# Optimization experiments

Measured on AMD Instinct MI355X. Metric: run time of the kernel, lower is better.

Reference implementation:

```python
import jax, jax.numpy as jnp
import numpy as np

EPS = 1e-8      # covariance regularizer (module-level `eps` in source repo)
ALPHA = 0.8     # style/content blend (module-level `alpha` in source repo)
SV_THRESH = 1e-5  # singular-value cutoff from the source


def _flatten(x):
    # x: [1, H, W, C] -> [C, H*W]
    xt = jnp.transpose(x[0], (2, 0, 1))  # C, H, W
    C = xt.shape[0]
    return xt.reshape(C, -1)


def _cov(f):
    # f: [C, N] already centered -> [C, C]
    C, N = f.shape
    return f @ f.T / (jnp.float32(N) - 1.0) + EPS * jnp.eye(C, dtype=f.dtype)


def _masked_pow(S, p):
    # Faithful to truncating columns with S <= 1e-5: zero their diag weight.
    mask = S > SV_THRESH
    S_safe = jnp.where(mask, S, 1.0)
    return jnp.where(mask, S_safe ** p, 0.0)


def setup_inputs() -> dict:
    key = jax.random.key(0)
    k1, k2 = jax.random.split(key)
    content = jax.random.normal(k1, (1, 128, 128, 512), dtype=jnp.float32)
    style = jax.random.normal(k2, (1, 128, 128, 512), dtype=jnp.float32)
    return {"content": content, "style": style}


def reference(content, style):
    H, W, C = content.shape[1], content.shape[2], content.shape[3]

    content_flat = _flatten(content)  # [C, Hc*Wc]
    style_flat = _flatten(style)      # [C, Hs*Ws]

    mc = content_flat.mean(axis=1, keepdims=True)
    fc = content_flat - mc
    ms = style_flat.mean(axis=1, keepdims=True)
    fs = style_flat - ms

    fcfc = _cov(fc)
    fsfs = _cov(fs)

    # tf.svd on a symmetric PSD matrix: S descending, U orthonormal.
    Uc, Sc, _ = jnp.linalg.svd(fcfc)
    Us, Ss, _ = jnp.linalg.svd(fsfs)

    # Whitening: Uc diag(Sc^-1/2) Uc^T (truncated cols == zeroed diag entries)
    Dc = _masked_pow(Sc, -0.5)
    whiten = (Uc * Dc[None, :]) @ Uc.T  # [C, C]
    fc_hat = whiten @ fc                # [C, N]

    # Coloring: Us diag(Ss^1/2) Us^T
    Ds = _masked_pow(Ss, 0.5)
    color = (Us * Ds[None, :]) @ Us.T
    fcs_hat = color @ fc_hat + ms

    blended = ALPHA * fcs_hat + (1.0 - ALPHA) * (fc + mc)  # [C, N]
    blended = blended.reshape(C, H, W)
    return jnp.transpose(blended, (1, 2, 0))[None]  # [1, H, W, C]
```

## Files before the change

kernel.cpp:

```cpp
#include <hip/hip_runtime.h>
#include <math.h>

#define NPIX 16384
#define CCH  512
#define MS   262144

typedef unsigned short u16;
typedef unsigned int u32;
typedef __attribute__((ext_vector_type(8))) short bf16x8;
typedef __attribute__((ext_vector_type(4))) float f32x4;

__device__ __forceinline__ u16 f2bf(float f) {
  u32 u = __builtin_bit_cast(u32, f);
  u += 0x7fffu + ((u >> 16) & 1u);
  return (u16)(u >> 16);
}
__device__ __forceinline__ float b2f(u16 h) {
  u32 u = ((u32)h) << 16;
  return __builtin_bit_cast(float, u);
}

typedef const __attribute__((address_space(1))) u32* gp_t;
typedef __attribute__((address_space(3))) u32* lp_t;
__device__ __forceinline__ void gl_lds16(const void* g, void* l) {
  __builtin_amdgcn_global_load_lds((gp_t)g, (lp_t)l, 16, 0, 0);
}

__device__ __forceinline__ void stage4(const u16* tile, size_t stride, int rl,
                                       int k0, u16* lds, int lane) {
  int lr = lane >> 4;
  int cg = (lane & 15) ^ ((rl + lr) & 15);
  gl_lds16(tile + (size_t)(rl + lr) * stride + k0 + cg * 8,
           lds + (size_t)rl * 128);
}
__device__ __forceinline__ bf16x8 fragld(const u16* lds, int row, int cl) {
  return *(const bf16x8*)&lds[(size_t)row * 128 + (size_t)((cl ^ (row & 15)) << 3)];
}

__device__ __forceinline__ void stage8_64(const u16* tile, size_t stride, int rl,
                                          int k0, u16* lds, int lane) {
  int lr = lane >> 3;
  int cg = (lane & 7) ^ ((rl + lr) & 7);
  gl_lds16(tile + (size_t)(rl + lr) * stride + k0 + cg * 8,
           lds + (size_t)rl * 64);
}
__device__ __forceinline__ bf16x8 fragld64(const u16* lds, int row, int cl) {
  return *(const bf16x8*)&lds[(size_t)row * 64 + (size_t)((cl ^ (row & 7)) << 3)];
}

__global__ __launch_bounds__(256) void prep_k(const float* __restrict__ Xc,
                                              const float* __restrict__ Xs,
                                              float* __restrict__ sums,
                                              u16* __restrict__ fct,
                                              u16* __restrict__ fcb) {
  int b = blockIdx.z;
  const float* X = b ? Xs : Xc;
  u16* outT = fct + (size_t)b * ((size_t)CCH * NPIX);
  __shared__ float T[64][65];
  __shared__ float red2[64][4];
  int n0 = blockIdx.x * 64, c0 = blockIdx.y * 64;
  int t = threadIdx.x;
  int cr = t & 15, nr = t >> 4;
  #pragma unroll
  for (int rr = 0; rr < 4; ++rr) {
    int n = nr + rr * 16;
    float4 v = *(const float4*)&X[(size_t)(n0 + n) * CCH + c0 + cr * 4];
    T[n][cr * 4 + 0] = v.x;
    T[n][cr * 4 + 1] = v.y;
    T[n][cr * 4 + 2] = v.z;
    T[n][cr * 4 + 3] = v.w;
    if (b == 0) {
      ushort4 q;
      q.x = f2bf(v.x); q.y = f2bf(v.y); q.z = f2bf(v.z); q.w = f2bf(v.w);
      *(ushort4*)&fcb[(size_t)(n0 + n) * CCH + c0 + cr * 4] = q;
    }
  }
  __syncthreads();
  int cl = t >> 2, np = (t & 3) * 16;
  size_t obase = (size_t)(c0 + cl) * NPIX + n0 + np;
  float s = 0.f;
  #pragma unroll
  for (int i = 0; i < 16; i += 4) {
    float v0 = T[np + i + 0][cl], v1 = T[np + i + 1][cl];
    float v2 = T[np + i + 2][cl], v3 = T[np + i + 3][cl];
    s += v0 + v1 + v2 + v3;
    ushort4 o;
    o.x = f2bf(v0); o.y = f2bf(v1); o.z = f2bf(v2); o.w = f2bf(v3);
    *(ushort4*)&outT[obase + i] = o;
  }
  red2[cl][t & 3] = s;
  __syncthreads();
  if (t < 64) {
    float cs = red2[t][0] + red2[t][1] + red2[t][2] + red2[t][3];
    atomicAdd(&sums[b * CCH + c0 + t], cs);
  }
}

__global__ __launch_bounds__(256, 2) void gram_part(const u16* __restrict__ fct,
                                                    float* __restrict__ Gp) {
  int kc = blockIdx.x;
  int pair = blockIdx.y;
  int b = blockIdx.z;
  int bi = pair >> 2, bj = pair & 3;
  const u16* Xb = fct + (size_t)b * ((size_t)CCH * NPIX);
  __shared__ u16 As[2][128 * 64];
  __shared__ u16 Bs[2][128 * 64];
  int tid = threadIdx.x, w = tid >> 6, lane = tid & 63;
  int qm = w & 1, qn = w >> 1;
  const u16* ssrc = (w < 2) ? Xb + (size_t)(bi * 128) * NPIX
                            : Xb + (size_t)(bj * 128) * NPIX;
  int rbase = (w & 1) * 64;
  f32x4 acc[4][4];
  #pragma unroll
  for (int t = 0; t < 4; ++t)
    #pragma unroll
    for (int u = 0; u < 4; ++u) acc[t][u] = (f32x4)(0.f);

  #pragma unroll
  for (int i = 0; i < 8; ++i)
    stage8_64(ssrc, NPIX, rbase + i * 8, kc * 1024, (w < 2) ? As[0] : Bs[0], lane);
  __syncthreads();

  for (int st = 0; st < 16; ++st) {
    int cur = st & 1;
    if (st < 15) {
      int k0n = kc * 1024 + (st + 1) * 64;
      #pragma unroll
      for (int i = 0; i < 8; ++i)
        stage8_64(ssrc, NPIX, rbase + i * 8, k0n,
                  (w < 2) ? As[cur ^ 1] : Bs[cur ^ 1], lane);
    }
    #pragma unroll
    for (int s = 0; s < 2; ++s) {
      int cl = s * 4 + (lane >> 4);
      bf16x8 a[4], bb[4];
      #pragma unroll
      for (int t = 0; t < 4; ++t) a[t] = fragld64(As[cur], qm * 64 + t * 16 + (lane & 15), cl);
      #pragma unroll
      for (int u = 0; u < 4; ++u) bb[u] = fragld64(Bs[cur], qn * 64 + u * 16 + (lane & 15), cl);
      #pragma unroll
      for (int t = 0; t < 4; ++t)
        #pragma unroll
        for (int u = 0; u < 4; ++u)
          acc[t][u] = __builtin_amdgcn_mfma_f32_16x16x32_bf16(a[t], bb[u], acc[t][u], 0, 0, 0);
    }
    __syncthreads();
  }
  size_t tbase = ((size_t)(b * 16 + kc) * 16 + pair) * 16384;
  #pragma unroll
  for (int t = 0; t < 4; ++t) {
    int row0 = qm * 64 + t * 16 + (lane >> 4) * 4;
    #pragma unroll
    for (int u = 0; u < 4; ++u) {
      int col = qn * 64 + u * 16 + (lane & 15);
      #pragma unroll
      for (int r4 = 0; r4 < 4; ++r4)
        Gp[tbase + (size_t)(row0 + r4) * 128 + col] = acc[t][u][r4];
    }
  }
}

__global__ __launch_bounds__(256) void gram_reduce(const float* __restrict__ Gp,
                                                   const float* __restrict__ sums,
                                                   float* __restrict__ cov,
                                                   float* __restrict__ rowsum) {
  int idx = blockIdx.x * 256 + threadIdx.x;
  int b = idx >> 18;
  int ij = idx & (MS - 1);
  int i = ij >> 9, j = ij & 511;
  int pair = ((i >> 7) << 2) | (j >> 7);
  int lij = ((i & 127) << 7) | (j & 127);
  size_t base = ((size_t)(b * 16) * 16 + pair) * 16384 + lij;
  float g = 0.f;
  #pragma unroll
  for (int kc = 0; kc < 16; ++kc)
    g += Gp[base + (size_t)kc * (16 * 16384)];
  const float* s = sums + b * CCH;
  float v = (g - s[i] * s[j] * (1.f / (float)NPIX)) * (1.f / (float)(NPIX - 1));
  if (i == j) v += 1e-8f;
  cov[idx] = v;
  __shared__ float red[256];
  int t = threadIdx.x;
  red[t] = fabsf(v);
  __syncthreads();
  for (int st = 128; st > 0; st >>= 1) {
    if (t < st) red[t] += red[t + st];
    __syncthreads();
  }
  if (t == 0) atomicAdd(&rowsum[b * CCH + i], red[0]);
}

__global__ __launch_bounds__(256) void nsinit_k(const float* __restrict__ cov,
                                                const float* __restrict__ rowsum,
                                                float* __restrict__ snorm,
                                                float* __restrict__ coef,
                                                u16* __restrict__ Anh,
                                                u16* __restrict__ Anl,
                                                u16* __restrict__ Z0) {
  __shared__ float red[256];
  int tid = threadIdx.x, blk = blockIdx.x;
  float m = fmaxf(rowsum[tid], rowsum[tid + 256]);
  red[tid] = m; __syncthreads();
  for (int s = 128; s > 0; s >>= 1) {
    if (tid < s) red[tid] = fmaxf(red[tid], red[tid + s]);
    __syncthreads();
  }
  float snc = red[0]; __syncthreads();
  m = fmaxf(rowsum[512 + tid], rowsum[768 + tid]);
  red[tid] = m; __syncthreads();
  for (int s = 128; s > 0; s >>= 1) {
    if (tid < s) red[tid] = fmaxf(red[tid], red[tid + s]);
    __syncthreads();
  }
  float sns = red[0];
  if (blk == 0 && tid == 0) {
    snorm[0] = snc; snorm[1] = sns;
    coef[0] = 0.8f * sqrtf(sns / snc);
  }
  int idx = blk * 256 + tid;
  int b = idx >> 18;
  int ij = idx & (MS - 1);
  int diag = (ij >> 9) == (ij & 511);
  float av = cov[idx] * (b ? 1.f / sns : 1.f / snc);
  u16 hi = f2bf(av);
  Anh[idx] = hi;
  Anl[idx] = f2bf(av - b2f(hi));
  float t0 = (diag ? 3.f - av : -av) * 0.70710678f;
  Z0[idx] = f2bf(t0);
}

struct MM16 {
  const u16* A[4];
  const u16* B[4];
  void* D[4];
  float scale, diag;
  int outFp32;
};

__global__ __launch_bounds__(256) void mm16_k(MM16 args) {
  int z = blockIdx.z;
  const u16* __restrict__ A = args.A[z];
  const u16* __restrict__ B = args.B[z];
  int bi = blockIdx.y, bj = blockIdx.x;
  __shared__ u16 As[2][64 * 128];
  __shared__ u16 Bs[2][64 * 128];
  int tid = threadIdx.x, w = tid >> 6, lane = tid & 63;
  int qm = w & 1, qn = w >> 1;
  const u16* ssrc = ((w < 2) ? A + (size_t)(bi * 64) * CCH : B + (size_t)(bj * 64) * CCH);
  int rbase = (w & 1) * 32;
  f32x4 acc[2][2];
  #pragma unroll
  for (int t = 0; t < 2; ++t)
    #pragma unroll
    for (int u = 0; u < 2; ++u) acc[t][u] = (f32x4)(0.f);

  #pragma unroll
  for (int i = 0; i < 8; ++i)
    stage4(ssrc, CCH, rbase + i * 4, 0, (w < 2) ? As[0] : Bs[0], lane);
  __syncthreads();

  for (int st = 0; st < 4; ++st) {
    int cur = st & 1;
    if (st < 3) {
      #pragma unroll
      for (int i = 0; i < 8; ++i)
        stage4(ssrc, CCH, rbase + i * 4, (st + 1) * 128,
               (w < 2) ? As[cur ^ 1] : Bs[cur ^ 1], lane);
    }
    #pragma unroll
    for (int s = 0; s < 4; ++s) {
      int cl = s * 4 + (lane >> 4);
      bf16x8 a[2], bb[2];
      #pragma unroll
      for (int t = 0; t < 2; ++t) a[t] = fragld(As[cur], qm * 32 + t * 16 + (lane & 15), cl);
      #pragma unroll
      for (int u = 0; u < 2; ++u) bb[u] = fragld(Bs[cur], qn * 32 + u * 16 + (lane & 15), cl);
      #pragma unroll
      for (int t = 0; t < 2; ++t)
        #pragma unroll
        for (int u = 0; u < 2; ++u)
          acc[t][u] = __builtin_amdgcn_mfma_f32_16x16x32_bf16(a[t], bb[u], acc[t][u], 0, 0, 0);
    }
    __syncthreads();
  }
  float sc = args.scale;
  #pragma unroll
  for (int t = 0; t < 2; ++t) {
    int row0 = bi * 64 + qm * 32 + t * 16 + (lane >> 4) * 4;
    #pragma unroll
    for (int u = 0; u < 2; ++u) {
      int col = bj * 64 + qn * 32 + u * 16 + (lane & 15);
      #pragma unroll
      for (int r4 = 0; r4 < 4; ++r4) {
        float v = sc * acc[t][u][r4];
        if (row0 + r4 == col) v += args.diag;
        size_t o = (size_t)(row0 + r4) * CCH + col;
        if (args.outFp32) ((float*)args.D[z])[o] = v;
        else ((u16*)args.D[z])[o] = f2bf(v);
      }
    }
  }
}

__global__ __launch_bounds__(256) void symsplit_k(const float* __restrict__ src,
                                                  u16* __restrict__ hi,
                                                  u16* __restrict__ lo) {
  int b = blockIdx.y;
  int ij = blockIdx.x * 256 + threadIdx.x;
  int i = ij >> 9, j = ij & 511;
  size_t base = (size_t)b * MS;
  float v = 0.5f * (src[base + ij] + src[base + (size_t)j * CCH + i]);
  u16 h = f2bf(v);
  hi[base + ij] = h;
  lo[base + ij] = f2bf(v - b2f(h));
}

struct MMS {
  const u16 *Ah[4], *Al[4], *Bh[4], *Bl[4];
  const u16 *Eh[4], *El[4];
  u16 *Dh[4], *Dl[4];
  float *D32[4];
  u16 *Db[4];
  float scale, beta;
  const float* coefPtr;
};

__global__ __launch_bounds__(256) void mmsplit_k(MMS args) {
  int z = blockIdx.z;
  int bi = blockIdx.y, bj = blockIdx.x;
  __shared__ u16 Ash[2][64 * 64], Asl[2][64 * 64];
  __shared__ u16 Bsh[2][64 * 64], Bsl[2][64 * 64];
  int tid = threadIdx.x, w = tid >> 6, lane = tid & 63;
  int qm = w & 1, qn = w >> 1;
  const u16* sp = (w == 0) ? args.Ah[z] : (w == 1) ? args.Al[z]
                : (w == 2) ? args.Bh[z] : args.Bl[z];
  const u16* ssrc = sp + (size_t)(((w < 2) ? bi : bj) * 64) * CCH;
  u16* sd0 = (w == 0) ? Ash[0] : (w == 1) ? Asl[0] : (w == 2) ? Bsh[0] : Bsl[0];
  u16* sd1 = (w == 0) ? Ash[1] : (w == 1) ? Asl[1] : (w == 2) ? Bsh[1] : Bsl[1];
  f32x4 acc[2][2];
  #pragma unroll
  for (int t = 0; t < 2; ++t)
    #pragma unroll
    for (int u = 0; u < 2; ++u) acc[t][u] = (f32x4)(0.f);

  #pragma unroll
  for (int i = 0; i < 8; ++i)
    stage8_64(ssrc, CCH, i * 8, 0, sd0, lane);
  __syncthreads();

  for (int st = 0; st < 8; ++st) {
    int cur = st & 1;
    if (st < 7) {
      u16* sdn = cur ? sd0 : sd1;
      #pragma unroll
      for (int i = 0; i < 8; ++i)
        stage8_64(ssrc, CCH, i * 8, (st + 1) * 64, sdn, lane);
    }
    #pragma unroll
    for (int s = 0; s < 2; ++s) {
      int cl = s * 4 + (lane >> 4);
      bf16x8 ah[2], al[2], bh[2], bl[2];
      #pragma unroll
      for (int t = 0; t < 2; ++t) {
        int row = qm * 32 + t * 16 + (lane & 15);
        ah[t] = fragld64(Ash[cur], row, cl);
        al[t] = fragld64(Asl[cur], row, cl);
      }
      #pragma unroll
      for (int u = 0; u < 2; ++u) {
        int row = qn * 32 + u * 16 + (lane & 15);
        bh[u] = fragld64(Bsh[cur], row, cl);
        bl[u] = fragld64(Bsl[cur], row, cl);
      }
      #pragma unroll
      for (int t = 0; t < 2; ++t)
        #pragma unroll
        for (int u = 0; u < 2; ++u) {
          acc[t][u] = __builtin_amdgcn_mfma_f32_16x16x32_bf16(ah[t], bh[u], acc[t][u], 0, 0, 0);
          acc[t][u] = __builtin_amdgcn_mfma_f32_16x16x32_bf16(ah[t], bl[u], acc[t][u], 0, 0, 0);
          acc[t][u] = __builtin_amdgcn_mfma_f32_16x16x32_bf16(al[t], bh[u], acc[t][u], 0, 0, 0);
        }
    }
    __syncthreads();
  }
  float sc = args.scale;
  if (args.coefPtr) sc *= *args.coefPtr;
  #pragma unroll
  for (int t = 0; t < 2; ++t) {
    int row0 = bi * 64 + qm * 32 + t * 16 + (lane >> 4) * 4;
    #pragma unroll
    for (int u = 0; u < 2; ++u) {
      int col = bj * 64 + qn * 32 + u * 16 + (lane & 15);
      #pragma unroll
      for (int r4 = 0; r4 < 4; ++r4) {
        size_t o = (size_t)(row0 + r4) * CCH + col;
        float v = sc * acc[t][u][r4];
        if (args.beta != 0.f) v += args.beta * (b2f(args.Eh[z][o]) + b2f(args.El[z][o]));
        if (args.D32[z]) args.D32[z][o] = v;
        if (args.Dh[z]) {
          u16 h = f2bf(v);
          args.Dh[z][o] = h;
          args.Dl[z][o] = f2bf(v - b2f(h));
        }
        if (args.Db[z]) args.Db[z][o] = f2bf(v);
      }
    }
  }
}

__global__ __launch_bounds__(256) void mconst_k(const u16* __restrict__ Mb,
                                                const float* __restrict__ sums,
                                                float* __restrict__ mconst) {
  int c = blockIdx.x * 8 + (threadIdx.x >> 5);
  int l = threadIdx.x & 31;
  float s = 0.f;
  #pragma unroll
  for (int k = 0; k < 16; ++k) {
    int j = l + 32 * k;
    s += b2f(Mb[(size_t)c * CCH + j]) * sums[j];
  }
  s += __shfl_down(s, 16, 32);
  s += __shfl_down(s, 8, 32);
  s += __shfl_down(s, 4, 32);
  s += __shfl_down(s, 2, 32);
  s += __shfl_down(s, 1, 32);
  if (l == 0) mconst[c] = (0.8f * sums[512 + c] - s) * (1.f / (float)NPIX);
}

__global__ __launch_bounds__(256) void apply_mfma(const u16* __restrict__ fcb,
                                                  const u16* __restrict__ Mb,
                                                  const float* __restrict__ mconst,
                                                  const float* __restrict__ X,
                                                  float* __restrict__ out) {
  int bi = blockIdx.y;
  int bj = blockIdx.x;
  __shared__ u16 As[2][128 * 64];
  __shared__ u16 Bs[2][128 * 64];
  int tid = threadIdx.x, w = tid >> 6, lane = tid & 63;
  int qm = w & 1, qn = w >> 1;
  const u16* ssrc = (w < 2) ? fcb + (size_t)(bi * 128) * CCH
                            : Mb + (size_t)(bj * 128) * CCH;
  int rbase = (w & 1) * 64;
  f32x4 acc[4][4];
  #pragma unroll
  for (int t = 0; t < 4; ++t)
    #pragma unroll
    for (int u = 0; u < 4; ++u) acc[t][u] = (f32x4)(0.f);

  #pragma unroll
  for (int i = 0; i < 8; ++i)
    stage8_64(ssrc, CCH, rbase + i * 8, 0, (w < 2) ? As[0] : Bs[0], lane);
  __syncthreads();

  for (int st = 0; st < 8; ++st) {
    int cur = st & 1;
    if (st < 7) {
      #pragma unroll
      for (int i = 0; i < 8; ++i)
        stage8_64(ssrc, CCH, rbase + i * 8, (st + 1) * 64,
                  (w < 2) ? As[cur ^ 1] : Bs[cur ^ 1], lane);
    }
    #pragma unroll
    for (int s = 0; s < 2; ++s) {
      int cl = s * 4 + (lane >> 4);
      bf16x8 a[4], bb[4];
      #pragma unroll
      for (int t = 0; t < 4; ++t) a[t] = fragld64(As[cur], qm * 64 + t * 16 + (lane & 15), cl);
      #pragma unroll
      for (int u = 0; u < 4; ++u) bb[u] = fragld64(Bs[cur], qn * 64 + u * 16 + (lane & 15), cl);
      #pragma unroll
      for (int t = 0; t < 4; ++t)
        #pragma unroll
        for (int u = 0; u < 4; ++u)
          acc[t][u] = __builtin_amdgcn_mfma_f32_16x16x32_bf16(a[t], bb[u], acc[t][u], 0, 0, 0);
    }
    __syncthreads();
  }
  #pragma unroll
  for (int t = 0; t < 4; ++t) {
    int row0 = bi * 128 + qm * 64 + t * 16 + (lane >> 4) * 4;
    #pragma unroll
    for (int u = 0; u < 4; ++u) {
      int col = bj * 128 + qn * 64 + u * 16 + (lane & 15);
      float cst = mconst[col];
      #pragma unroll
      for (int r4 = 0; r4 < 4; ++r4) {
        size_t o = (size_t)(row0 + r4) * CCH + col;
        out[o] = acc[t][u][r4] + cst + 0.2f * X[o];
      }
    }
  }
}

extern "C" void kernel_launch(void* const* d_in, const int* in_sizes, int n_in,
                              void* d_out, int out_size, void* d_ws, size_t ws_size,
                              hipStream_t stream) {
  const float* Xc = (const float*)d_in[0];
  const float* Xs = (const float*)d_in[1];
  float* out = (float*)d_out;

  float* f = (float*)d_ws;
  float* sums   = f;
  float* rowsum = f + 1024;
  float* cov    = f + 2048 + 2 * MS;
  float* snorm  = cov + 2 * MS;
  float* coef   = snorm + 8;
  float* mconst = coef + 8;
  float* Zf     = mconst + 512;

  float* Gp = (float*)d_out;

  u16* h   = (u16*)(Zf + 2 * MS);
  u16* fct = h;
  u16* fcb = h + (size_t)2 * CCH * NPIX;
  const size_t B2 = 2 * MS;
  u16* Anh  = fct + 0 * B2;
  u16* Anl  = fct + 1 * B2;
  u16* Y1   = fct + 2 * B2;
  u16* Ya   = fct + 3 * B2;
  u16* Z0   = fct + 4 * B2;
  u16* Z1   = fct + 5 * B2;
  u16* Tb   = fct + 6 * B2;
  u16* Zfsh = fct + 7 * B2;
  u16* Zfsl = fct + 8 * B2;
  u16* Ph   = fct + 9 * B2;
  u16* Pl   = fct + 10 * B2;
  u16* Qh   = fct + 11 * B2;
  u16* Ql   = fct + 12 * B2;
  u16* Zrsh = fct + 13 * B2;
  u16* Zrsl = fct + 14 * B2;
  u16* W2h  = fct + 15 * B2;
  u16* W2l  = W2h + MS;
  u16* Mb   = W2l + MS;

  hipMemsetAsync(d_ws, 0, 2048 * sizeof(float), stream);

  prep_k<<<dim3(256, 8, 2), 256, 0, stream>>>(Xc, Xs, sums, fct, fcb);
  gram_part<<<dim3(16, 16, 2), 256, 0, stream>>>(fct, Gp);
  gram_reduce<<<2048, 256, 0, stream>>>(Gp, sums, cov, rowsum);
  nsinit_k<<<2048, 256, 0, stream>>>(cov, rowsum, snorm, coef, Anh, Anl, Z0);

  {
    MM16 y1{};
    y1.A[0] = Anh;      y1.B[0] = Z0;      y1.D[0] = Y1;
    y1.A[1] = Anh + MS; y1.B[1] = Z0 + MS; y1.D[1] = Y1 + MS;
    y1.scale = 1.f; y1.diag = 0.f; y1.outFp32 = 0;
    mm16_k<<<dim3(8, 8, 2), 256, 0, stream>>>(y1);
  }
  {
    MM16 t{};
    t.A[0] = Z0;      t.B[0] = Y1;      t.D[0] = Tb;
    t.A[1] = Z0 + MS; t.B[1] = Y1 + MS; t.D[1] = Tb + MS;
    t.scale = -1.f; t.diag = 3.f; t.outFp32 = 0;
    mm16_k<<<dim3(8, 8, 2), 256, 0, stream>>>(t);
  }
  {
    MM16 yz{};
    yz.A[0] = Y1;      yz.B[0] = Tb;      yz.D[0] = Ya;
    yz.A[1] = Y1 + MS; yz.B[1] = Tb + MS; yz.D[1] = Ya + MS;
    yz.A[2] = Tb;      yz.B[2] = Z0;      yz.D[2] = Z1;
    yz.A[3] = Tb + MS; yz.B[3] = Z0 + MS; yz.D[3] = Z1 + MS;
    yz.scale = 0.5f; yz.diag = 0.f; yz.outFp32 = 0;
    mm16_k<<<dim3(8, 8, 4), 256, 0, stream>>>(yz);
  }
  {
    MM16 t{};
    t.A[0] = Z1;      t.B[0] = Ya;      t.D[0] = Tb;
    t.A[1] = Z1 + MS; t.B[1] = Ya + MS; t.D[1] = Tb + MS;
    t.scale = -1.f; t.diag = 3.f; t.outFp32 = 0;
    mm16_k<<<dim3(8, 8, 2), 256, 0, stream>>>(t);
  }
  {
    MM16 yz{};
    yz.A[0] = Ya;      yz.B[0] = Tb;      yz.D[0] = Y1;
    yz.A[1] = Ya + MS; yz.B[1] = Tb + MS; yz.D[1] = Y1 + MS;
    yz.A[2] = Tb;      yz.B[2] = Z1;      yz.D[2] = Z0;
    yz.A[3] = Tb + MS; yz.B[3] = Z1 + MS; yz.D[3] = Z0 + MS;
    yz.scale = 0.5f; yz.diag = 0.f; yz.outFp32 = 0;
    mm16_k<<<dim3(8, 8, 4), 256, 0, stream>>>(yz);
  }
  {
    MM16 t{};
    t.A[0] = Z0;      t.B[0] = Y1;      t.D[0] = Tb;
    t.A[1] = Z0 + MS; t.B[1] = Y1 + MS; t.D[1] = Tb + MS;
    t.scale = -1.f; t.diag = 3.f; t.outFp32 = 0;
    mm16_k<<<dim3(8, 8, 2), 256, 0, stream>>>(t);
  }
  {
    MM16 zf{};
    zf.A[0] = Tb;      zf.B[0] = Z0;      zf.D[0] = Zf;
    zf.A[1] = Tb + MS; zf.B[1] = Z0 + MS; zf.D[1] = Zf + MS;
    zf.scale = 0.5f; zf.diag = 0.f; zf.outFp32 = 1;
    mm16_k<<<dim3(8, 8, 2), 256, 0, stream>>>(zf);
  }

  symsplit_k<<<dim3(1024, 2), 256, 0, stream>>>(Zf, Zfsh, Zfsl);

  MMS pq{};
  for (int b = 0; b < 2; ++b) {
    pq.Ah[b] = Zfsh + b * MS; pq.Al[b] = Zfsl + b * MS;
    pq.Bh[b] = Anh + b * MS;  pq.Bl[b] = Anl + b * MS;
    pq.Dh[b] = Ph + b * MS;   pq.Dl[b] = Pl + b * MS;
    pq.Ah[2 + b] = Zfsh + b * MS; pq.Al[2 + b] = Zfsl + b * MS;
    pq.Bh[2 + b] = Zfsh + b * MS; pq.Bl[2 + b] = Zfsl + b * MS;
    pq.Dh[2 + b] = Qh + b * MS;   pq.Dl[2 + b] = Ql + b * MS;
  }
  pq.scale = 1.f;
  mmsplit_k<<<dim3(8, 8, 4), 256, 0, stream>>>(pq);

  MMS zr{};
  for (int b = 0; b < 2; ++b) {
    zr.Ah[b] = Ph + b * MS;   zr.Al[b] = Pl + b * MS;
    zr.Bh[b] = Qh + b * MS;   zr.Bl[b] = Ql + b * MS;
    zr.Eh[b] = Zfsh + b * MS; zr.El[b] = Zfsl + b * MS;
    zr.D32[b] = Zf + b * MS;
  }
  zr.scale = -0.5f; zr.beta = 1.5f;
  mmsplit_k<<<dim3(8, 8, 2), 256, 0, stream>>>(zr);

  symsplit_k<<<dim3(1024, 2), 256, 0, stream>>>(Zf, Zrsh, Zrsl);

  MMS wv{};
  wv.Ah[0] = Anh + MS;  wv.Al[0] = Anl + MS;
  wv.Bh[0] = Zrsh + MS; wv.Bl[0] = Zrsl + MS;
  wv.Dh[0] = W2h; wv.Dl[0] = W2l;
  wv.scale = 1.f;
  mmsplit_k<<<dim3(8, 8, 1), 256, 0, stream>>>(wv);

  MMS mv{};
  mv.Ah[0] = W2h;  mv.Al[0] = W2l;
  mv.Bh[0] = Zrsh; mv.Bl[0] = Zrsl;
  mv.Db[0] = Mb;
  mv.scale = 1.f; mv.coefPtr = coef;
  mmsplit_k<<<dim3(8, 8, 1), 256, 0, stream>>>(mv);

  mconst_k<<<64, 256, 0, stream>>>(Mb, sums, mconst);
  apply_mfma<<<dim3(4, 128), 256, 0, stream>>>(fcb, Mb, mconst, Xc, out);
}
```

Before: 275.5 us.

## Fuse Newton-Schulz matmuls with symmetrization into upper-triangle tile kernels

Replaces the fp32 matmul followed by a separate symmetrize-and-split kernel with kernels that compute only upper-triangular 64x64 tile pairs. Each block computes both the (i,j) and (j,i) tiles, averages them through LDS, emits the hi/lo bf16 split, and writes both mirrored locations. This removes two fp32 intermediate round trips and two kernel launches. The cost is double MFMA work per block over only 36 blocks instead of 64, so each block carries more serial work.

After: 283.4 us. 2.9% more time.

```diff
diff --git a/kernel.cpp b/kernel.cpp
--- a/kernel.cpp
+++ b/kernel.cpp
@@ -29,8 +29,8 @@
 __device__ __forceinline__ void stage4(const u16* tile, size_t stride, int rl,
                                        int k0, u16* lds, int lane) {
   int lr = lane >> 4;
-  int cg = (lane & 15) ^ ((rl + lr) & 15);
-  gl_lds16(tile + (size_t)(rl + lr) * stride + k0 + cg * 8,
+  int cg2 = (lane & 15) ^ ((rl + lr) & 15);
+  gl_lds16(tile + (size_t)(rl + lr) * stride + k0 + cg2 * 8,
            lds + (size_t)rl * 128);
 }
 __device__ __forceinline__ bf16x8 fragld(const u16* lds, int row, int cl) {
@@ -40,8 +40,8 @@
 __device__ __forceinline__ void stage8_64(const u16* tile, size_t stride, int rl,
                                           int k0, u16* lds, int lane) {
   int lr = lane >> 3;
-  int cg = (lane & 7) ^ ((rl + lr) & 7);
-  gl_lds16(tile + (size_t)(rl + lr) * stride + k0 + cg * 8,
+  int cg2 = (lane & 7) ^ ((rl + lr) & 7);
+  gl_lds16(tile + (size_t)(rl + lr) * stride + k0 + cg2 * 8,
            lds + (size_t)rl * 64);
 }
 __device__ __forceinline__ bf16x8 fragld64(const u16* lds, int row, int cl) {
@@ -302,17 +302,106 @@
   }
 }
 
-__global__ __launch_bounds__(256) void symsplit_k(const float* __restrict__ src,
-                                                  u16* __restrict__ hi,
-                                                  u16* __restrict__ lo) {
-  int b = blockIdx.y;
-  int ij = blockIdx.x * 256 + threadIdx.x;
-  int i = ij >> 9, j = ij & 511;
-  size_t base = (size_t)b * MS;
-  float v = 0.5f * (src[base + ij] + src[base + (size_t)j * CCH + i]);
-  u16 h = f2bf(v);
-  hi[base + ij] = h;
-  lo[base + ij] = f2bf(v - b2f(h));
+__global__ __launch_bounds__(256, 2) void zfsym_k(const u16* __restrict__ Tb,
+                                                  const u16* __restrict__ Z0,
+                                                  u16* __restrict__ Oh_,
+                                                  u16* __restrict__ Ol_) {
+  int z = blockIdx.z;
+  int p = blockIdx.x;
+  int bi = 0, pp = p;
+  while (pp >= 8 - bi) { pp -= 8 - bi; ++bi; }
+  int bj = bi + pp;
+  const u16* A = Tb + (size_t)z * MS;
+  const u16* B = Z0 + (size_t)z * MS;
+  u16* Oh = Oh_ + (size_t)z * MS;
+  u16* Ol = Ol_ + (size_t)z * MS;
+  __shared__ u16 smem[32768];
+  int tid = threadIdx.x, w = tid >> 6, lane = tid & 63;
+  int qm = w & 1, qn = w >> 1;
+  const u16* ssrc = (w == 0) ? A + (size_t)(bi * 64) * CCH
+                  : (w == 1) ? B + (size_t)(bj * 64) * CCH
+                  : (w == 2) ? A + (size_t)(bj * 64) * CCH
+                             : B + (size_t)(bi * 64) * CCH;
+  u16* sbase = smem + w * 8192;
+  f32x4 acc1[2][2], acc2[2][2];
+  #pragma unroll
+  for (int t = 0; t < 2; ++t)
+    #pragma unroll
+    for (int u = 0; u < 2; ++u) { acc1[t][u] = (f32x4)(0.f); acc2[t][u] = (f32x4)(0.f); }
+
+  #pragma unroll
+  for (int i = 0; i < 8; ++i) stage8_64(ssrc, CCH, i * 8, 0, sbase, lane);
+  __syncthreads();
+  for (int st = 0; st < 8; ++st) {
+    int cur = st & 1;
+    if (st < 7) {
+      u16* sdst = sbase + (cur ^ 1) * 4096;
+      #pragma unroll
+      for (int i = 0; i < 8; ++i) stage8_64(ssrc, CCH, i * 8, (st + 1) * 64, sdst, lane);
+    }
+    u16* P0 = smem + 0 * 8192 + cur * 4096;
+    u16* P1 = smem + 1 * 8192 + cur * 4096;
+    u16* P2 = smem + 2 * 8192 + cur * 4096;
+    u16* P3 = smem + 3 * 8192 + cur * 4096;
+    #pragma unroll
+    for (int s = 0; s < 2; ++s) {
+      int cl = s * 4 + (lane >> 4);
+      bf16x8 a1[2], b1[2], a2[2], b2[2];
+      #pragma unroll
+      for (int t = 0; t < 2; ++t) a1[t] = fragld64(P0, qm * 32 + t * 16 + (lane & 15), cl);
+      #pragma unroll
+      for (int u = 0; u < 2; ++u) b1[u] = fragld64(P1, qn * 32 + u * 16 + (lane & 15), cl);
+      #pragma unroll
+      for (int t = 0; t < 2; ++t)
+        #pragma unroll
+        for (int u = 0; u < 2; ++u)
+          acc1[t][u] = __builtin_amdgcn_mfma_f32_16x16x32_bf16(a1[t], b1[u], acc1[t][u], 0, 0, 0);
+      #pragma unroll
+      for (int t = 0; t < 2; ++t) a2[t] = fragld64(P2, qm * 32 + t * 16 + (lane & 15), cl);
+      #pragma unroll
+      for (int u = 0; u < 2; ++u) b2[u] = fragld64(P3, qn * 32 + u * 16 + (lane & 15), cl);
+      #pragma unroll
+      for (int t = 0; t < 2; ++t)
+        #pragma unroll
+        for (int u = 0; u < 2; ++u)
+          acc2[t][u] = __builtin_amdgcn_mfma_f32_16x16x32_bf16(a2[t], b2[u], acc2[t][u], 0, 0, 0);
+    }
+    __syncthreads();
+  }
+  const float sc = 0.5f;
+  float* fs = (float*)smem;
+  #pragma unroll
+  for (int t = 0; t < 2; ++t) {
+    int r20 = qm * 32 + t * 16 + (lane >> 4) * 4;
+    #pragma unroll
+    for (int u = 0; u < 2; ++u) {
+      int c2 = qn * 32 + u * 16 + (lane & 15);
+      #pragma unroll
+      for (int r4 = 0; r4 < 4; ++r4)
+        fs[(r20 + r4) * 65 + c2] = sc * acc2[t][u][r4];
+    }
+  }
+  __syncthreads();
+  #pragma unroll
+  for (int t = 0; t < 2; ++t) {
+    int r0 = qm * 32 + t * 16 + (lane >> 4) * 4;
+    #pragma unroll
+    for (int u = 0; u < 2; ++u) {
+      int c = qn * 32 + u * 16 + (lane & 15);
+      #pragma unroll
+      for (int r4 = 0; r4 < 4; ++r4) {
+        int r = r0 + r4;
+        float v = 0.5f * (sc * acc1[t][u][r4] + fs[c * 65 + r]);
+        u16 hh = f2bf(v), ll = f2bf(v - b2f(hh));
+        size_t o1 = (size_t)(bi * 64 + r) * CCH + (bj * 64 + c);
+        Oh[o1] = hh; Ol[o1] = ll;
+        if (bi != bj) {
+          size_t o2 = (size_t)(bj * 64 + c) * CCH + (bi * 64 + r);
+          Oh[o2] = hh; Ol[o2] = ll;
+        }
+      }
+    }
+  }
 }
 
 struct MMS {
@@ -403,6 +492,141 @@
           args.Dl[z][o] = f2bf(v - b2f(h));
         }
         if (args.Db[z]) args.Db[z][o] = f2bf(v);
+      }
+    }
+  }
+}
+
+__global__ __launch_bounds__(256, 2) void zrsym_k(const u16* __restrict__ Ph_,
+                                                  const u16* __restrict__ Pl_,
+                                                  const u16* __restrict__ Qh_,
+                                                  const u16* __restrict__ Ql_,
+                                                  const u16* __restrict__ Eh_,
+                                                  const u16* __restrict__ El_,
+                                                  u16* __restrict__ Oh_,
+                                                  u16* __restrict__ Ol_) {
+  int z = blockIdx.z;
+  int p = blockIdx.x;
+  int bi = 0, pp = p;
+  while (pp >= 8 - bi) { pp -= 8 - bi; ++bi; }
+  int bj = bi + pp;
+  const u16* Ph = Ph_ + (size_t)z * MS;
+  const u16* Pl = Pl_ + (size_t)z * MS;
+  const u16* Qh = Qh_ + (size_t)z * MS;
+  const u16* Ql = Ql_ + (size_t)z * MS;
+  const u16* Eh = Eh_ + (size_t)z * MS;
+  const u16* El = El_ + (size_t)z * MS;
+  u16* Oh = Oh_ + (size_t)z * MS;
+  u16* Ol = Ol_ + (size_t)z * MS;
+  __shared__ u16 smem[32768];
+  int tid = threadIdx.x, w = tid >> 6, lane = tid & 63;
+  int qm = w & 1, qn = w >> 1;
+  const u16* s1 = (w == 0) ? Ph + (size_t)(bi * 64) * CCH
+                : (w == 1) ? Pl + (size_t)(bi * 64) * CCH
+                : (w == 2) ? Qh + (size_t)(bj * 64) * CCH
+                           : Ql + (size_t)(bj * 64) * CCH;
+  const u16* s2 = (w == 0) ? Ph + (size_t)(bj * 64) * CCH
+                : (w == 1) ? Pl + (size_t)(bj * 64) * CCH
+                : (w == 2) ? Qh + (size_t)(bi * 64) * CCH
+                           : Ql + (size_t)(bi * 64) * CCH;
+  u16* d1 = smem + w * 4096;
+  u16* d2 = smem + (w + 4) * 4096;
+  f32x4 acc1[2][2], acc2[2][2];
+  #pragma unroll
+  for (int t = 0; t < 2; ++t)
+    #pragma unroll
+    for (int u = 0; u < 2; ++u) { acc1[t][u] = (f32x4)(0.f); acc2[t][u] = (f32x4)(0.f); }
+
+  for (int st = 0; st < 8; ++st) {
+    __syncthreads();
+    #pragma unroll
+    for (int i = 0; i < 8; ++i) stage8_64(s1, CCH, i * 8, st * 64, d1, lane);
+    #pragma unroll
+    for (int i = 0; i < 8; ++i) stage8_64(s2, CCH, i * 8, st * 64, d2, lane);
+    __syncthreads();
+    #pragma unroll
+    for (int s = 0; s < 2; ++s) {
+      int cl = s * 4 + (lane >> 4);
+      bf16x8 ah[2], al[2], bh[2], bl[2];
+      #pragma unroll
+      for (int t = 0; t < 2; ++t) {
+        int row = qm * 32 + t * 16 + (lane & 15);
+        ah[t] = fragld64(smem + 0 * 4096, row, cl);
+        al[t] = fragld64(smem + 1 * 4096, row, cl);
+      }
+      #pragma unroll
+      for (int u = 0; u < 2; ++u) {
+        int row = qn * 32 + u * 16 + (lane & 15);
+        bh[u] = fragld64(smem + 2 * 4096, row, cl);
+        bl[u] = fragld64(smem + 3 * 4096, row, cl);
+      }
+      #pragma unroll
+      for (int t = 0; t < 2; ++t)
+        #pragma unroll
+        for (int u = 0; u < 2; ++u) {
+          acc1[t][u] = __builtin_amdgcn_mfma_f32_16x16x32_bf16(ah[t], bh[u], acc1[t][u], 0, 0, 0);
+          acc1[t][u] = __builtin_amdgcn_mfma_f32_16x16x32_bf16(ah[t], bl[u], acc1[t][u], 0, 0, 0);
+          acc1[t][u] = __builtin_amdgcn_mfma_f32_16x16x32_bf16(al[t], bh[u], acc1[t][u], 0, 0, 0);
+        }
+      #pragma unroll
+      for (int t = 0; t < 2; ++t) {
+        int row = qm * 32 + t * 16 + (lane & 15);
+        ah[t] = fragld64(smem + 4 * 4096, row, cl);
+        al[t] = fragld64(smem + 5 * 4096, row, cl);
+      }
+      #pragma unroll
+      for (int u = 0; u < 2; ++u) {
+        int row = qn * 32 + u * 16 + (lane & 15);
+        bh[u] = fragld64(smem + 6 * 4096, row, cl);
+        bl[u] = fragld64(smem + 7 * 4096, row, cl);
+      }
+      #pragma unroll
+      for (int t = 0; t < 2; ++t)
+        #pragma unroll
+        for (int u = 0; u < 2; ++u) {
+          acc2[t][u] = __builtin_amdgcn_mfma_f32_16x16x32_bf16(ah[t], bh[u], acc2[t][u], 0, 0, 0);
+          acc2[t][u] = __builtin_amdgcn_mfma_f32_16x16x32_bf16(ah[t], bl[u], acc2[t][u], 0, 0, 0);
+          acc2[t][u] = __builtin_amdgcn_mfma_f32_16x16x32_bf16(al[t], bh[u], acc2[t][u], 0, 0, 0);
+        }
+    }
+  }
+  const float sc = -0.5f, beta = 1.5f;
+  float* fs = (float*)smem;
+  __syncthreads();
+  #pragma unroll
+  for (int t = 0; t < 2; ++t) {
+    int r20 = qm * 32 + t * 16 + (lane >> 4) * 4;
+    #pragma unroll
+    for (int u = 0; u < 2; ++u) {
+      int c2 = qn * 32 + u * 16 + (lane & 15);
+      #pragma unroll
+      for (int r4 = 0; r4 < 4; ++r4) {
+        int r2 = r20 + r4;
+        size_t o2e = (size_t)(bj * 64 + r2) * CCH + (bi * 64 + c2);
+        float z2 = sc * acc2[t][u][r4] + beta * (b2f(Eh[o2e]) + b2f(El[o2e]));
+        fs[r2 * 65 + c2] = z2;
+      }
+    }
+  }
+  __syncthreads();
+  #pragma unroll
+  for (int t = 0; t < 2; ++t) {
+    int r0 = qm * 32 + t * 16 + (lane >> 4) * 4;
+    #pragma unroll
+    for (int u = 0; u < 2; ++u) {
+      int c = qn * 32 + u * 16 + (lane & 15);
+      #pragma unroll
+      for (int r4 = 0; r4 < 4; ++r4) {
+        int r = r0 + r4;
+        size_t o1 = (size_t)(bi * 64 + r) * CCH + (bj * 64 + c);
+        float z1 = sc * acc1[t][u][r4] + beta * (b2f(Eh[o1]) + b2f(El[o1]));
+        float v = 0.5f * (z1 + fs[c * 65 + r]);
+        u16 hh = f2bf(v), ll = f2bf(v - b2f(hh));
+        Oh[o1] = hh; Ol[o1] = ll;
+        if (bi != bj) {
+          size_t o2 = (size_t)(bj * 64 + c) * CCH + (bi * 64 + r);
+          Oh[o2] = hh; Ol[o2] = ll;
+        }
       }
     }
   }
@@ -586,15 +810,8 @@
     t.scale = -1.f; t.diag = 3.f; t.outFp32 = 0;
     mm16_k<<<dim3(8, 8, 2), 256, 0, stream>>>(t);
   }
-  {
-    MM16 zf{};
-    zf.A[0] = Tb;      zf.B[0] = Z0;      zf.D[0] = Zf;
-    zf.A[1] = Tb + MS; zf.B[1] = Z0 + MS; zf.D[1] = Zf + MS;
-    zf.scale = 0.5f; zf.diag = 0.f; zf.outFp32 = 1;
-    mm16_k<<<dim3(8, 8, 2), 256, 0, stream>>>(zf);
-  }
-
-  symsplit_k<<<dim3(1024, 2), 256, 0, stream>>>(Zf, Zfsh, Zfsl);
+
+  zfsym_k<<<dim3(36, 1, 2), 256, 0, stream>>>(Tb, Z0, Zfsh, Zfsl);
 
   MMS pq{};
   for (int b = 0; b < 2; ++b) {
@@ -608,17 +825,7 @@
   pq.scale = 1.f;
   mmsplit_k<<<dim3(8, 8, 4), 256, 0, stream>>>(pq);
 
-  MMS zr{};
-  for (int b = 0; b < 2; ++b) {
-    zr.Ah[b] = Ph + b * MS;   zr.Al[b] = Pl + b * MS;
-    zr.Bh[b] = Qh + b * MS;   zr.Bl[b] = Ql + b * MS;
-    zr.Eh[b] = Zfsh + b * MS; zr.El[b] = Zfsl + b * MS;
-    zr.D32[b] = Zf + b * MS;
-  }
-  zr.scale = -0.5f; zr.beta = 1.5f;
-  mmsplit_k<<<dim3(8, 8, 2), 256, 0, stream>>>(zr);
-
-  symsplit_k<<<dim3(1024, 2), 256, 0, stream>>>(Zf, Zrsh, Zrsl);
+  zrsym_k<<<dim3(36, 1, 2), 256, 0, stream>>>(Ph, Pl, Qh, Ql, Zfsh, Zfsl, Zrsh, Zrsl);
 
   MMS wv{};
   wv.Ah[0] = Anh + MS;  wv.Al[0] = Anl + MS;
```
